# Performance work log

Hardware: AMD Instinct MI355X
Metric: run time of the kernel (lower is better)

The kernel has to match this reference:

```python
import jax, jax.numpy as jnp
import numpy as np

B, N, T, D = 32, 1024, 64, 32  # latent_dim = D


def setup_inputs() -> dict:
    key = jax.random.key(0)
    ks = jax.random.split(key, 12)
    s = 0.1
    return {
        "spatial_nodes": jax.random.normal(ks[0], (B, N, D), jnp.float32),
        "temporal_nodes": jax.random.normal(ks[1], (B, T, D), jnp.float32),
        # st MLP: Linear(2D -> D), Sigmoid, Linear(D -> 1). Weights stored (in, out).
        "st_w1": jax.random.normal(ks[2], (2 * D, D), jnp.float32) * s,
        "st_b1": jax.random.normal(ks[3], (D,), jnp.float32) * s,
        "st_w2": jax.random.normal(ks[4], (D, 1), jnp.float32) * s,
        "st_b2": jax.random.normal(ks[5], (1,), jnp.float32) * s,
        "ts_w1": jax.random.normal(ks[6], (2 * D, D), jnp.float32) * s,
        "ts_b1": jax.random.normal(ks[7], (D,), jnp.float32) * s,
        "ts_w2": jax.random.normal(ks[8], (D, 1), jnp.float32) * s,
        "ts_b2": jax.random.normal(ks[9], (1,), jnp.float32) * s,
    }


def _sub_graph(x1, x2, w1, b1, w2, b2):
    # Faithful to Linear(concat(x1_tile, x2_tile)) but without materializing
    # the tiled/concatenated [B, N1, N2, 2D] tensor: split w1 by input half.
    d = x1.shape[-1]
    a = x1 @ w1[:d]          # [B, N1, D]
    b = x2 @ w1[d:]          # [B, N2, D]
    h = jax.nn.sigmoid(a[:, :, None, :] + b[:, None, :, :] + b1)  # [B, N1, N2, D]
    return jnp.einsum('bnmd,do->bnm', h, w2) + b2[0]               # [B, N1, N2]


def reference(spatial_nodes, temporal_nodes,
              st_w1, st_b1, st_w2, st_b2,
              ts_w1, ts_b1, ts_w2, ts_b2):
    n = spatial_nodes.shape[1]
    node_embs = jnp.concatenate([spatial_nodes, temporal_nodes], axis=1)  # [B, N+T, D]
    adj = jnp.einsum('bnf,bmf->bnm', node_embs, node_embs)                # [B, N+T, N+T]
    st_adj = _sub_graph(spatial_nodes, temporal_nodes, st_w1, st_b1, st_w2, st_b2)
    ts_adj = _sub_graph(temporal_nodes, spatial_nodes, ts_w1, ts_b1, ts_w2, ts_b2)
    adj = adj.at[:, :n, n:].set(st_adj)
    adj = adj.at[:, n:, :n].set(ts_adj)
    adj = jnp.tanh(jax.nn.relu(adj))
    return adj
```

## Files before the change

### kernel.cpp

```cpp
#include <hip/hip_runtime.h>

namespace {
constexpr int kB = 32;
constexpr int kN = 1024;
constexpr int kT = 64;
constexpr int kD = 32;
constexpr int kM = 1088;

constexpr int BLK_NN = kB * 8 * 8;
constexpr int BLK_ST = kB * 16;
constexpr int BLK_TS = kB * 16;
constexpr int BLK_TT = kB;
constexpr int BLK_TOTAL = BLK_NN + BLK_ST + BLK_TS + BLK_TT;

struct SMemGram128 {
  float A[128][36];
  float Bt[32][132];
};
struct SMemGram64 {
  float A[64][36];
  float Bt[32][68];
};
struct SMemMLP {
  union {
    struct { float raw1[64][36]; float raw2[64][36]; } r;
    struct { float EA[64][36]; float EBt[32][68]; } e;
  } u;
  float w1[64][32];
  float w2v[32];
  float b1v[32];
  float b2v;
};
union SMem { SMemGram128 g; SMemGram64 g64; SMemMLP m; };
}

__device__ __forceinline__ float tanh_relu(float x) {
  if (x <= 0.f) return 0.f;
  float e = __expf(2.f * x);
  return 1.f - 2.f * __builtin_amdgcn_rcpf(e + 1.f);
}

__global__ void __launch_bounds__(256)
adj_kernel(const float* __restrict__ sp, const float* __restrict__ tp,
           const float* __restrict__ st_w1, const float* __restrict__ st_b1,
           const float* __restrict__ st_w2, const float* __restrict__ st_b2,
           const float* __restrict__ ts_w1, const float* __restrict__ ts_b1,
           const float* __restrict__ ts_w2, const float* __restrict__ ts_b2,
           float* __restrict__ out) {
  __shared__ SMem sm;
  const int bid = blockIdx.x;
  const int tid = threadIdx.x;
  const int tx = tid & 15;
  const int ty = tid >> 4;

  if (bid < BLK_NN) {
    const int b = bid >> 6;
    const int t = bid & 63;
    const int r0 = (t >> 3) * 128;
    const int c0 = (t & 7) * 128;
    const float* rowp = sp + ((size_t)b * kN + r0) * kD;
    const float* colp = sp + ((size_t)b * kN + c0) * kD;
    for (int q = tid; q < 1024; q += 256) {
      const int r = q >> 3, c = (q & 7) * 4;
      *(float4*)&sm.g.A[r][c] = ((const float4*)rowp)[q];
      const float4 w = ((const float4*)colp)[q];
      sm.g.Bt[c + 0][r] = w.x;
      sm.g.Bt[c + 1][r] = w.y;
      sm.g.Bt[c + 2][r] = w.z;
      sm.g.Bt[c + 3][r] = w.w;
    }
    __syncthreads();
    float acc[8][8] = {};
    #pragma unroll
    for (int k4 = 0; k4 < 8; ++k4) {
      float4 a0[4], a1[4];
      #pragma unroll
      for (int i = 0; i < 4; ++i) {
        a0[i] = *(const float4*)&sm.g.A[ty * 4 + i][k4 * 4];
        a1[i] = *(const float4*)&sm.g.A[64 + ty * 4 + i][k4 * 4];
      }
      #pragma unroll
      for (int kk = 0; kk < 4; ++kk) {
        const int k = k4 * 4 + kk;
        const float4 b0 = *(const float4*)&sm.g.Bt[k][tx * 4];
        const float4 b1 = *(const float4*)&sm.g.Bt[k][64 + tx * 4];
        #pragma unroll
        for (int i = 0; i < 4; ++i) {
          const float av0 = (&a0[i].x)[kk];
          const float av1 = (&a1[i].x)[kk];
          acc[i][0] = fmaf(av0, b0.x, acc[i][0]);
          acc[i][1] = fmaf(av0, b0.y, acc[i][1]);
          acc[i][2] = fmaf(av0, b0.z, acc[i][2]);
          acc[i][3] = fmaf(av0, b0.w, acc[i][3]);
          acc[i][4] = fmaf(av0, b1.x, acc[i][4]);
          acc[i][5] = fmaf(av0, b1.y, acc[i][5]);
          acc[i][6] = fmaf(av0, b1.z, acc[i][6]);
          acc[i][7] = fmaf(av0, b1.w, acc[i][7]);
          acc[4 + i][0] = fmaf(av1, b0.x, acc[4 + i][0]);
          acc[4 + i][1] = fmaf(av1, b0.y, acc[4 + i][1]);
          acc[4 + i][2] = fmaf(av1, b0.z, acc[4 + i][2]);
          acc[4 + i][3] = fmaf(av1, b0.w, acc[4 + i][3]);
          acc[4 + i][4] = fmaf(av1, b1.x, acc[4 + i][4]);
          acc[4 + i][5] = fmaf(av1, b1.y, acc[4 + i][5]);
          acc[4 + i][6] = fmaf(av1, b1.z, acc[4 + i][6]);
          acc[4 + i][7] = fmaf(av1, b1.w, acc[4 + i][7]);
        }
      }
    }
    const size_t base = (size_t)b * kM * kM + (size_t)c0 + tx * 4;
    #pragma unroll
    for (int h = 0; h < 2; ++h) {
      #pragma unroll
      for (int i = 0; i < 4; ++i) {
        const int r = r0 + h * 64 + ty * 4 + i;
        const float* a = acc[h * 4 + i];
        float4 o0, o1;
        o0.x = tanh_relu(a[0]); o0.y = tanh_relu(a[1]);
        o0.z = tanh_relu(a[2]); o0.w = tanh_relu(a[3]);
        o1.x = tanh_relu(a[4]); o1.y = tanh_relu(a[5]);
        o1.z = tanh_relu(a[6]); o1.w = tanh_relu(a[7]);
        *(float4*)&out[base + (size_t)r * kM] = o0;
        *(float4*)&out[base + (size_t)r * kM + 64] = o1;
      }
    }
  } else if (bid >= BLK_NN + BLK_ST + BLK_TS) {
    const int b = bid - (BLK_NN + BLK_ST + BLK_TS);
    const float* rowp = tp + (size_t)b * kT * kD;
    for (int q = tid; q < 512; q += 256) {
      const int r = q >> 3, c = (q & 7) * 4;
      const float4 v = ((const float4*)rowp)[q];
      *(float4*)&sm.g64.A[r][c] = v;
      sm.g64.Bt[c + 0][r] = v.x;
      sm.g64.Bt[c + 1][r] = v.y;
      sm.g64.Bt[c + 2][r] = v.z;
      sm.g64.Bt[c + 3][r] = v.w;
    }
    __syncthreads();
    float acc[4][4] = {};
    #pragma unroll
    for (int k4 = 0; k4 < 8; ++k4) {
      float4 a4[4];
      #pragma unroll
      for (int i = 0; i < 4; ++i)
        a4[i] = *(const float4*)&sm.g64.A[ty * 4 + i][k4 * 4];
      #pragma unroll
      for (int kk = 0; kk < 4; ++kk) {
        const float4 b4 = *(const float4*)&sm.g64.Bt[k4 * 4 + kk][tx * 4];
        #pragma unroll
        for (int i = 0; i < 4; ++i) {
          const float av = (&a4[i].x)[kk];
          acc[i][0] = fmaf(av, b4.x, acc[i][0]);
          acc[i][1] = fmaf(av, b4.y, acc[i][1]);
          acc[i][2] = fmaf(av, b4.z, acc[i][2]);
          acc[i][3] = fmaf(av, b4.w, acc[i][3]);
        }
      }
    }
    const size_t base = (size_t)b * kM * kM + (size_t)kN + tx * 4;
    #pragma unroll
    for (int i = 0; i < 4; ++i) {
      const int r = kN + ty * 4 + i;
      float4 o;
      o.x = tanh_relu(acc[i][0]);
      o.y = tanh_relu(acc[i][1]);
      o.z = tanh_relu(acc[i][2]);
      o.w = tanh_relu(acc[i][3]);
      *(float4*)&out[base + (size_t)r * kM] = o;
    }
  } else {
    int i = bid - BLK_NN;
    int b, r0, c0;
    const float *rowp, *colp, *w1, *b1, *w2, *b2;
    if (i < BLK_ST) {
      b = i >> 4;
      r0 = (i & 15) * 64; c0 = kN;
      rowp = sp + ((size_t)b * kN + r0) * kD;
      colp = tp + (size_t)b * kT * kD;
      w1 = st_w1; b1 = st_b1; w2 = st_w2; b2 = st_b2;
    } else {
      i -= BLK_ST;
      b = i >> 4;
      r0 = kN; c0 = (i & 15) * 64;
      rowp = tp + (size_t)b * kT * kD;
      colp = sp + ((size_t)b * kN + c0) * kD;
      w1 = ts_w1; b1 = ts_b1; w2 = ts_w2; b2 = ts_b2;
    }
    for (int q = tid; q < 512; q += 256) {
      const int r = q >> 3, c = (q & 7) * 4;
      *(float4*)&sm.m.u.r.raw1[r][c] = ((const float4*)rowp)[q];
      *(float4*)&sm.m.u.r.raw2[r][c] = ((const float4*)colp)[q];
      ((float4*)sm.m.w1)[q] = ((const float4*)w1)[q];
    }
    if (tid < kD) { sm.m.w2v[tid] = w2[tid]; sm.m.b1v[tid] = b1[tid]; }
    if (tid == 0) sm.m.b2v = b2[0];
    __syncthreads();
    const int pr = tid >> 2;
    const int d0 = (tid & 3) * 8;
    float pa[8], pb[8];
    #pragma unroll
    for (int q = 0; q < 8; ++q) { pa[q] = 0.f; pb[q] = sm.m.b1v[d0 + q]; }
    #pragma unroll 4
    for (int k = 0; k < kD; ++k) {
      const float s1 = sm.m.u.r.raw1[pr][k];
      const float s2 = sm.m.u.r.raw2[pr][k];
      #pragma unroll
      for (int q = 0; q < 8; ++q) {
        pa[q] = fmaf(s1, sm.m.w1[k][d0 + q], pa[q]);
        pb[q] = fmaf(s2, sm.m.w1[kD + k][d0 + q], pb[q]);
      }
    }
    const float b2s = sm.m.b2v;
    __syncthreads();
    #pragma unroll
    for (int q = 0; q < 8; ++q) {
      sm.m.u.e.EA[pr][d0 + q] = __expf(-pa[q]);
      sm.m.u.e.EBt[d0 + q][pr] = __expf(-pb[q]);
    }
    __syncthreads();
    float acc[4][4];
    #pragma unroll
    for (int ii = 0; ii < 4; ++ii)
      #pragma unroll
      for (int jj = 0; jj < 4; ++jj) acc[ii][jj] = b2s;
    #pragma unroll
    for (int d4 = 0; d4 < 8; ++d4) {
      float4 ea4[4];
      #pragma unroll
      for (int ii = 0; ii < 4; ++ii)
        ea4[ii] = *(const float4*)&sm.m.u.e.EA[ty * 4 + ii][d4 * 4];
      #pragma unroll
      for (int dd = 0; dd < 4; ++dd) {
        const int d = d4 * 4 + dd;
        const float4 eb4 = *(const float4*)&sm.m.u.e.EBt[d][tx * 4];
        const float w2d = sm.m.w2v[d];
        #pragma unroll
        for (int ii = 0; ii < 4; ++ii) {
          const float eav = (&ea4[ii].x)[dd];
          acc[ii][0] = fmaf(w2d, __builtin_amdgcn_rcpf(fmaf(eav, eb4.x, 1.f)), acc[ii][0]);
          acc[ii][1] = fmaf(w2d, __builtin_amdgcn_rcpf(fmaf(eav, eb4.y, 1.f)), acc[ii][1]);
          acc[ii][2] = fmaf(w2d, __builtin_amdgcn_rcpf(fmaf(eav, eb4.z, 1.f)), acc[ii][2]);
          acc[ii][3] = fmaf(w2d, __builtin_amdgcn_rcpf(fmaf(eav, eb4.w, 1.f)), acc[ii][3]);
        }
      }
    }
    const size_t base = (size_t)b * kM * kM + (size_t)c0 + tx * 4;
    #pragma unroll
    for (int ii = 0; ii < 4; ++ii) {
      const int r = r0 + ty * 4 + ii;
      float4 o;
      o.x = tanh_relu(acc[ii][0]);
      o.y = tanh_relu(acc[ii][1]);
      o.z = tanh_relu(acc[ii][2]);
      o.w = tanh_relu(acc[ii][3]);
      *(float4*)&out[base + (size_t)r * kM] = o;
    }
  }
}

extern "C" void kernel_launch(void* const* d_in, const int* in_sizes, int n_in,
                              void* d_out, int out_size, void* d_ws, size_t ws_size,
                              hipStream_t stream) {
  const float* sp    = (const float*)d_in[0];
  const float* tp    = (const float*)d_in[1];
  const float* st_w1 = (const float*)d_in[2];
  const float* st_b1 = (const float*)d_in[3];
  const float* st_w2 = (const float*)d_in[4];
  const float* st_b2 = (const float*)d_in[5];
  const float* ts_w1 = (const float*)d_in[6];
  const float* ts_b1 = (const float*)d_in[7];
  const float* ts_w2 = (const float*)d_in[8];
  const float* ts_b2 = (const float*)d_in[9];
  float* out = (float*)d_out;
  (void)in_sizes; (void)n_in; (void)out_size; (void)d_ws; (void)ws_size;
  adj_kernel<<<dim3(BLK_TOTAL), dim3(256), 0, stream>>>(
      sp, tp, st_w1, st_b1, st_w2, st_b2, ts_w1, ts_b1, ts_w2, ts_b2, out);
}
```

Baseline: 220.0 us.

## Split fused kernel into separate Gram and sigmoid-MLP kernels, restructure inner loops

Splits the single heterogeneous kernel into a Gram-matrix kernel (NN and TT blocks) and an MLP kernel (ST and TS blocks), launched back to back on the same stream. Each kernel now gets its own register and LDS budget instead of the union of all branches, which could raise occupancy. The inner loops are reordered to load B vectors once per k4 and stream A rows, and the MLP projection uses float4 weight loads. tanh_relu becomes branchless via fmaxf. The cost is a second launch and the loss of overlap between the two block types.

```diff
diff --git a/kernel.cpp b/kernel.cpp
--- a/kernel.cpp
+++ b/kernel.cpp
@@ -8,19 +8,13 @@
 constexpr int kM = 1088;
 
 constexpr int BLK_NN = kB * 8 * 8;
+constexpr int BLK_TT = kB;
+constexpr int BLK_GRAM = BLK_NN + BLK_TT;
 constexpr int BLK_ST = kB * 16;
-constexpr int BLK_TS = kB * 16;
-constexpr int BLK_TT = kB;
-constexpr int BLK_TOTAL = BLK_NN + BLK_ST + BLK_TS + BLK_TT;
-
-struct SMemGram128 {
-  float A[128][36];
-  float Bt[32][132];
-};
-struct SMemGram64 {
-  float A[64][36];
-  float Bt[32][68];
-};
+constexpr int BLK_MLP = 2 * BLK_ST;
+
+struct SMemGram128 { float A[128][36]; float Bt[32][132]; };
+struct SMemGram64  { float A[64][36];  float Bt[32][68];  };
 struct SMemMLP {
   union {
     struct { float raw1[64][36]; float raw2[64][36]; } r;
@@ -31,23 +25,30 @@
   float b1v[32];
   float b2v;
 };
-union SMem { SMemGram128 g; SMemGram64 g64; SMemMLP m; };
-}
+}
+
+#define FMA4(ACC, AV, B, C)            \
+  ACC = fmaf(AV.x, B[0].C, ACC);       \
+  ACC = fmaf(AV.y, B[1].C, ACC);       \
+  ACC = fmaf(AV.z, B[2].C, ACC);       \
+  ACC = fmaf(AV.w, B[3].C, ACC);
+
+#define SIGSTEP(AROW, EAV, EBD, W2D)                                            \
+  AROW[0] = fmaf(W2D, __builtin_amdgcn_rcpf(fmaf(EAV, EBD.x, 1.f)), AROW[0]);   \
+  AROW[1] = fmaf(W2D, __builtin_amdgcn_rcpf(fmaf(EAV, EBD.y, 1.f)), AROW[1]);   \
+  AROW[2] = fmaf(W2D, __builtin_amdgcn_rcpf(fmaf(EAV, EBD.z, 1.f)), AROW[2]);   \
+  AROW[3] = fmaf(W2D, __builtin_amdgcn_rcpf(fmaf(EAV, EBD.w, 1.f)), AROW[3]);
 
 __device__ __forceinline__ float tanh_relu(float x) {
-  if (x <= 0.f) return 0.f;
-  float e = __expf(2.f * x);
+  const float xp = fmaxf(x, 0.f);
+  const float e = __expf(2.f * xp);
   return 1.f - 2.f * __builtin_amdgcn_rcpf(e + 1.f);
 }
 
 __global__ void __launch_bounds__(256)
-adj_kernel(const float* __restrict__ sp, const float* __restrict__ tp,
-           const float* __restrict__ st_w1, const float* __restrict__ st_b1,
-           const float* __restrict__ st_w2, const float* __restrict__ st_b2,
-           const float* __restrict__ ts_w1, const float* __restrict__ ts_b1,
-           const float* __restrict__ ts_w2, const float* __restrict__ ts_b2,
-           float* __restrict__ out) {
-  __shared__ SMem sm;
+gram_kernel(const float* __restrict__ sp, const float* __restrict__ tp,
+            float* __restrict__ out) {
+  __shared__ union { SMemGram128 g; SMemGram64 g64; } sm;
   const int bid = blockIdx.x;
   const int tid = threadIdx.x;
   const int tx = tid & 15;
@@ -73,58 +74,40 @@
     float acc[8][8] = {};
     #pragma unroll
     for (int k4 = 0; k4 < 8; ++k4) {
-      float4 a0[4], a1[4];
-      #pragma unroll
-      for (int i = 0; i < 4; ++i) {
-        a0[i] = *(const float4*)&sm.g.A[ty * 4 + i][k4 * 4];
-        a1[i] = *(const float4*)&sm.g.A[64 + ty * 4 + i][k4 * 4];
+      float4 b0[4], b1[4];
+      #pragma unroll
+      for (int kk = 0; kk < 4; ++kk) {
+        b0[kk] = *(const float4*)&sm.g.Bt[k4 * 4 + kk][tx * 4];
+        b1[kk] = *(const float4*)&sm.g.Bt[k4 * 4 + kk][64 + tx * 4];
       }
       #pragma unroll
-      for (int kk = 0; kk < 4; ++kk) {
-        const int k = k4 * 4 + kk;
-        const float4 b0 = *(const float4*)&sm.g.Bt[k][tx * 4];
-        const float4 b1 = *(const float4*)&sm.g.Bt[k][64 + tx * 4];
-        #pragma unroll
-        for (int i = 0; i < 4; ++i) {
-          const float av0 = (&a0[i].x)[kk];
-          const float av1 = (&a1[i].x)[kk];
-          acc[i][0] = fmaf(av0, b0.x, acc[i][0]);
-          acc[i][1] = fmaf(av0, b0.y, acc[i][1]);
-          acc[i][2] = fmaf(av0, b0.z, acc[i][2]);
-          acc[i][3] = fmaf(av0, b0.w, acc[i][3]);
-          acc[i][4] = fmaf(av0, b1.x, acc[i][4]);
-          acc[i][5] = fmaf(av0, b1.y, acc[i][5]);
-          acc[i][6] = fmaf(av0, b1.z, acc[i][6]);
-          acc[i][7] = fmaf(av0, b1.w, acc[i][7]);
-          acc[4 + i][0] = fmaf(av1, b0.x, acc[4 + i][0]);
-          acc[4 + i][1] = fmaf(av1, b0.y, acc[4 + i][1]);
-          acc[4 + i][2] = fmaf(av1, b0.z, acc[4 + i][2]);
-          acc[4 + i][3] = fmaf(av1, b0.w, acc[4 + i][3]);
-          acc[4 + i][4] = fmaf(av1, b1.x, acc[4 + i][4]);
-          acc[4 + i][5] = fmaf(av1, b1.y, acc[4 + i][5]);
-          acc[4 + i][6] = fmaf(av1, b1.z, acc[4 + i][6]);
-          acc[4 + i][7] = fmaf(av1, b1.w, acc[4 + i][7]);
-        }
+      for (int i = 0; i < 8; ++i) {
+        const int row = (i & 4) * 16 + ty * 4 + (i & 3);
+        const float4 a = *(const float4*)&sm.g.A[row][k4 * 4];
+        FMA4(acc[i][0], a, b0, x)
+        FMA4(acc[i][1], a, b0, y)
+        FMA4(acc[i][2], a, b0, z)
+        FMA4(acc[i][3], a, b0, w)
+        FMA4(acc[i][4], a, b1, x)
+        FMA4(acc[i][5], a, b1, y)
+        FMA4(acc[i][6], a, b1, z)
+        FMA4(acc[i][7], a, b1, w)
       }
     }
     const size_t base = (size_t)b * kM * kM + (size_t)c0 + tx * 4;
     #pragma unroll
-    for (int h = 0; h < 2; ++h) {
-      #pragma unroll
-      for (int i = 0; i < 4; ++i) {
-        const int r = r0 + h * 64 + ty * 4 + i;
-        const float* a = acc[h * 4 + i];
-        float4 o0, o1;
-        o0.x = tanh_relu(a[0]); o0.y = tanh_relu(a[1]);
-        o0.z = tanh_relu(a[2]); o0.w = tanh_relu(a[3]);
-        o1.x = tanh_relu(a[4]); o1.y = tanh_relu(a[5]);
-        o1.z = tanh_relu(a[6]); o1.w = tanh_relu(a[7]);
-        *(float4*)&out[base + (size_t)r * kM] = o0;
-        *(float4*)&out[base + (size_t)r * kM + 64] = o1;
-      }
-    }
-  } else if (bid >= BLK_NN + BLK_ST + BLK_TS) {
-    const int b = bid - (BLK_NN + BLK_ST + BLK_TS);
+    for (int i = 0; i < 8; ++i) {
+      const int r = r0 + (i & 4) * 16 + ty * 4 + (i & 3);
+      float4 o0, o1;
+      o0.x = tanh_relu(acc[i][0]); o0.y = tanh_relu(acc[i][1]);
+      o0.z = tanh_relu(acc[i][2]); o0.w = tanh_relu(acc[i][3]);
+      o1.x = tanh_relu(acc[i][4]); o1.y = tanh_relu(acc[i][5]);
+      o1.z = tanh_relu(acc[i][6]); o1.w = tanh_relu(acc[i][7]);
+      *(float4*)&out[base + (size_t)r * kM] = o0;
+      *(float4*)&out[base + (size_t)r * kM + 64] = o1;
+    }
+  } else {
+    const int b = bid - BLK_NN;
     const float* rowp = tp + (size_t)b * kT * kD;
     for (int q = tid; q < 512; q += 256) {
       const int r = q >> 3, c = (q & 7) * 4;
@@ -139,21 +122,17 @@
     float acc[4][4] = {};
     #pragma unroll
     for (int k4 = 0; k4 < 8; ++k4) {
-      float4 a4[4];
-      #pragma unroll
-      for (int i = 0; i < 4; ++i)
-        a4[i] = *(const float4*)&sm.g64.A[ty * 4 + i][k4 * 4];
-      #pragma unroll
-      for (int kk = 0; kk < 4; ++kk) {
-        const float4 b4 = *(const float4*)&sm.g64.Bt[k4 * 4 + kk][tx * 4];
-        #pragma unroll
-        for (int i = 0; i < 4; ++i) {
-          const float av = (&a4[i].x)[kk];
-          acc[i][0] = fmaf(av, b4.x, acc[i][0]);
-          acc[i][1] = fmaf(av, b4.y, acc[i][1]);
-          acc[i][2] = fmaf(av, b4.z, acc[i][2]);
-          acc[i][3] = fmaf(av, b4.w, acc[i][3]);
-        }
+      float4 b4[4];
+      #pragma unroll
+      for (int kk = 0; kk < 4; ++kk)
+        b4[kk] = *(const float4*)&sm.g64.Bt[k4 * 4 + kk][tx * 4];
+      #pragma unroll
+      for (int i = 0; i < 4; ++i) {
+        const float4 a = *(const float4*)&sm.g64.A[ty * 4 + i][k4 * 4];
+        FMA4(acc[i][0], a, b4, x)
+        FMA4(acc[i][1], a, b4, y)
+        FMA4(acc[i][2], a, b4, z)
+        FMA4(acc[i][3], a, b4, w)
       }
     }
     const size_t base = (size_t)b * kM * kM + (size_t)kN + tx * 4;
@@ -167,93 +146,113 @@
       o.w = tanh_relu(acc[i][3]);
       *(float4*)&out[base + (size_t)r * kM] = o;
     }
+  }
+}
+
+__global__ void __launch_bounds__(256)
+mlp_kernel(const float* __restrict__ sp, const float* __restrict__ tp,
+           const float* __restrict__ st_w1, const float* __restrict__ st_b1,
+           const float* __restrict__ st_w2, const float* __restrict__ st_b2,
+           const float* __restrict__ ts_w1, const float* __restrict__ ts_b1,
+           const float* __restrict__ ts_w2, const float* __restrict__ ts_b2,
+           float* __restrict__ out) {
+  __shared__ SMemMLP sm;
+  const int bid = blockIdx.x;
+  const int tid = threadIdx.x;
+  const int tx = tid & 15;
+  const int ty = tid >> 4;
+
+  int b, r0, c0;
+  const float *rowp, *colp, *w1, *b1, *w2, *b2;
+  if (bid < BLK_ST) {
+    b = bid >> 4;
+    r0 = (bid & 15) * 64; c0 = kN;
+    rowp = sp + ((size_t)b * kN + r0) * kD;
+    colp = tp + (size_t)b * kT * kD;
+    w1 = st_w1; b1 = st_b1; w2 = st_w2; b2 = st_b2;
   } else {
-    int i = bid - BLK_NN;
-    int b, r0, c0;
-    const float *rowp, *colp, *w1, *b1, *w2, *b2;
-    if (i < BLK_ST) {
-      b = i >> 4;
-      r0 = (i & 15) * 64; c0 = kN;
-      rowp = sp + ((size_t)b * kN + r0) * kD;
-      colp = tp + (size_t)b * kT * kD;
-      w1 = st_w1; b1 = st_b1; w2 = st_w2; b2 = st_b2;
-    } else {
-      i -= BLK_ST;
-      b = i >> 4;
-      r0 = kN; c0 = (i & 15) * 64;
-      rowp = tp + (size_t)b * kT * kD;
-      colp = sp + ((size_t)b * kN + c0) * kD;
-      w1 = ts_w1; b1 = ts_b1; w2 = ts_w2; b2 = ts_b2;
-    }
-    for (int q = tid; q < 512; q += 256) {
-      const int r = q >> 3, c = (q & 7) * 4;
-      *(float4*)&sm.m.u.r.raw1[r][c] = ((const float4*)rowp)[q];
-      *(float4*)&sm.m.u.r.raw2[r][c] = ((const float4*)colp)[q];
-      ((float4*)sm.m.w1)[q] = ((const float4*)w1)[q];
-    }
-    if (tid < kD) { sm.m.w2v[tid] = w2[tid]; sm.m.b1v[tid] = b1[tid]; }
-    if (tid == 0) sm.m.b2v = b2[0];
-    __syncthreads();
-    const int pr = tid >> 2;
-    const int d0 = (tid & 3) * 8;
-    float pa[8], pb[8];
-    #pragma unroll
-    for (int q = 0; q < 8; ++q) { pa[q] = 0.f; pb[q] = sm.m.b1v[d0 + q]; }
-    #pragma unroll 4
-    for (int k = 0; k < kD; ++k) {
-      const float s1 = sm.m.u.r.raw1[pr][k];
-      const float s2 = sm.m.u.r.raw2[pr][k];
-      #pragma unroll
-      for (int q = 0; q < 8; ++q) {
-        pa[q] = fmaf(s1, sm.m.w1[k][d0 + q], pa[q]);
-        pb[q] = fmaf(s2, sm.m.w1[kD + k][d0 + q], pb[q]);
-      }
-    }
-    const float b2s = sm.m.b2v;
-    __syncthreads();
-    #pragma unroll
-    for (int q = 0; q < 8; ++q) {
-      sm.m.u.e.EA[pr][d0 + q] = __expf(-pa[q]);
-      sm.m.u.e.EBt[d0 + q][pr] = __expf(-pb[q]);
-    }
-    __syncthreads();
-    float acc[4][4];
+    const int i = bid - BLK_ST;
+    b = i >> 4;
+    r0 = kN; c0 = (i & 15) * 64;
+    rowp = tp + (size_t)b * kT * kD;
+    colp = sp + ((size_t)b * kN + c0) * kD;
+    w1 = ts_w1; b1 = ts_b1; w2 = ts_w2; b2 = ts_b2;
+  }
+  for (int q = tid; q < 512; q += 256) {
+    const int r = q >> 3, c = (q & 7) * 4;
+    *(float4*)&sm.u.r.raw1[r][c] = ((const float4*)rowp)[q];
+    *(float4*)&sm.u.r.raw2[r][c] = ((const float4*)colp)[q];
+    ((float4*)sm.w1)[q] = ((const float4*)w1)[q];
+  }
+  if (tid < kD) { sm.w2v[tid] = w2[tid]; sm.b1v[tid] = b1[tid]; }
+  if (tid == 0) sm.b2v = b2[0];
+  __syncthreads();
+  const int pr = tid >> 2;
+  const int d0 = (tid & 3) * 8;
+  float pa[8], pb[8];
+  #pragma unroll
+  for (int q = 0; q < 8; ++q) { pa[q] = 0.f; pb[q] = sm.b1v[d0 + q]; }
+  for (int k = 0; k < kD; ++k) {
+    const float s1 = sm.u.r.raw1[pr][k];
+    const float s2 = sm.u.r.raw2[pr][k];
+    const float4 wa0 = *(const float4*)&sm.w1[k][d0];
+    const float4 wa1 = *(const float4*)&sm.w1[k][d0 + 4];
+    const float4 wb0 = *(const float4*)&sm.w1[kD + k][d0];
+    const float4 wb1 = *(const float4*)&sm.w1[kD + k][d0 + 4];
+    pa[0] = fmaf(s1, wa0.x, pa[0]); pa[1] = fmaf(s1, wa0.y, pa[1]);
+    pa[2] = fmaf(s1, wa0.z, pa[2]); pa[3] = fmaf(s1, wa0.w, pa[3]);
+    pa[4] = fmaf(s1, wa1.x, pa[4]); pa[5] = fmaf(s1, wa1.y, pa[5]);
+    pa[6] = fmaf(s1, wa1.z, pa[6]); pa[7] = fmaf(s1, wa1.w, pa[7]);
+    pb[0] = fmaf(s2, wb0.x, pb[0]); pb[1] = fmaf(s2, wb0.y, pb[1]);
+    pb[2] = fmaf(s2, wb0.z, pb[2]); pb[3] = fmaf(s2, wb0.w, pb[3]);
+    pb[4] = fmaf(s2, wb1.x, pb[4]); pb[5] = fmaf(s2, wb1.y, pb[5]);
+    pb[6] = fmaf(s2, wb1.z, pb[6]); pb[7] = fmaf(s2, wb1.w, pb[7]);
+  }
+  const float b2s = sm.b2v;
+  __syncthreads();
+  #pragma unroll
+  for (int q = 0; q < 8; ++q) {
+    sm.u.e.EA[pr][d0 + q] = __expf(-pa[q]);
+    sm.u.e.EBt[d0 + q][pr] = __expf(-pb[q]);
+  }
+  __syncthreads();
+  float acc[4][4];
+  #pragma unroll
+  for (int ii = 0; ii < 4; ++ii) {
+    acc[ii][0] = b2s; acc[ii][1] = b2s; acc[ii][2] = b2s; acc[ii][3] = b2s;
+  }
+  #pragma unroll
+  for (int d4 = 0; d4 < 8; ++d4) {
+    float4 ea[4];
     #pragma unroll
     for (int ii = 0; ii < 4; ++ii)
-      #pragma unroll
-      for (int jj = 0; jj < 4; ++jj) acc[ii][jj] = b2s;
-    #pragma unroll
-    for (int d4 = 0; d4 < 8; ++d4) {
-      float4 ea4[4];
-      #pragma unroll
-      for (int ii = 0; ii < 4; ++ii)
-        ea4[ii] = *(const float4*)&sm.m.u.e.EA[ty * 4 + ii][d4 * 4];
-      #pragma unroll
-      for (int dd = 0; dd < 4; ++dd) {
-        const int d = d4 * 4 + dd;
-        const float4 eb4 = *(const float4*)&sm.m.u.e.EBt[d][tx * 4];
-        const float w2d = sm.m.w2v[d];
-        #pragma unroll
-        for (int ii = 0; ii < 4; ++ii) {
-          const float eav = (&ea4[ii].x)[dd];
-          acc[ii][0] = fmaf(w2d, __builtin_amdgcn_rcpf(fmaf(eav, eb4.x, 1.f)), acc[ii][0]);
-          acc[ii][1] = fmaf(w2d, __builtin_amdgcn_rcpf(fmaf(eav, eb4.y, 1.f)), acc[ii][1]);
-          acc[ii][2] = fmaf(w2d, __builtin_amdgcn_rcpf(fmaf(eav, eb4.z, 1.f)), acc[ii][2]);
-          acc[ii][3] = fmaf(w2d, __builtin_amdgcn_rcpf(fmaf(eav, eb4.w, 1.f)), acc[ii][3]);
-        }
-      }
-    }
-    const size_t base = (size_t)b * kM * kM + (size_t)c0 + tx * 4;
+      ea[ii] = *(const float4*)&sm.u.e.EA[ty * 4 + ii][d4 * 4];
+    const float4 eb0 = *(const float4*)&sm.u.e.EBt[d4 * 4 + 0][tx * 4];
+    const float4 eb1 = *(const float4*)&sm.u.e.EBt[d4 * 4 + 1][tx * 4];
+    const float4 eb2 = *(const float4*)&sm.u.e.EBt[d4 * 4 + 2][tx * 4];
+    const float4 eb3 = *(const float4*)&sm.u.e.EBt[d4 * 4 + 3][tx * 4];
+    const float w20 = sm.w2v[d4 * 4 + 0];
+    const float w21 = sm.w2v[d4 * 4 + 1];
+    const float w22 = sm.w2v[d4 * 4 + 2];
+    const float w23 = sm.w2v[d4 * 4 + 3];
     #pragma unroll
     for (int ii = 0; ii < 4; ++ii) {
-      const int r = r0 + ty * 4 + ii;
-      float4 o;
-      o.x = tanh_relu(acc[ii][0]);
-      o.y = tanh_relu(acc[ii][1]);
-      o.z = tanh_relu(acc[ii][2]);
-      o.w = tanh_relu(acc[ii][3]);
-      *(float4*)&out[base + (size_t)r * kM] = o;
-    }
+      SIGSTEP(acc[ii], ea[ii].x, eb0, w20)
+      SIGSTEP(acc[ii], ea[ii].y, eb1, w21)
+      SIGSTEP(acc[ii], ea[ii].z, eb2, w22)
+      SIGSTEP(acc[ii], ea[ii].w, eb3, w23)
+    }
+  }
+  const size_t base = (size_t)b * kM * kM + (size_t)c0 + tx * 4;
+  #pragma unroll
+  for (int ii = 0; ii < 4; ++ii) {
+    const int r = r0 + ty * 4 + ii;
+    float4 o;
+    o.x = tanh_relu(acc[ii][0]);
+    o.y = tanh_relu(acc[ii][1]);
+    o.z = tanh_relu(acc[ii][2]);
+    o.w = tanh_relu(acc[ii][3]);
+    *(float4*)&out[base + (size_t)r * kM] = o;
   }
 }
 
@@ -272,6 +271,7 @@
   const float* ts_b2 = (const float*)d_in[9];
   float* out = (float*)d_out;
   (void)in_sizes; (void)n_in; (void)out_size; (void)d_ws; (void)ws_size;
-  adj_kernel<<<dim3(BLK_TOTAL), dim3(256), 0, stream>>>(
+  gram_kernel<<<dim3(BLK_GRAM), dim3(256), 0, stream>>>(sp, tp, out);
+  mlp_kernel<<<dim3(BLK_MLP), dim3(256), 0, stream>>>(
       sp, tp, st_w1, st_b1, st_w2, st_b2, ts_w1, ts_b1, ts_w2, ts_b2, out);
 }
```

Result: no change. 219.5 us (-0.3%).
